# Optimization experiments

Measured on AMD Instinct MI355X. Metric: run time of the kernel, lower is better.

The kernel has to match this reference:

```python
import jax, jax.numpy as jnp
import numpy as np

B, LQ, LK, D = 16, 2048, 2048, 64
TEMPERATURE = 8.0


def setup_inputs() -> dict:
    key = jax.random.key(0)
    kq, kk, kv, kt, km = jax.random.split(key, 5)
    q = jax.random.normal(kq, (B, LQ, D), dtype=jnp.float32)
    k = jax.random.normal(kk, (B, LK, D), dtype=jnp.float32)
    v = jax.random.normal(kv, (B, LK, D), dtype=jnp.float32)
    # time differences are positive
    time_diff = jax.random.uniform(kt, (B, LQ, LK), dtype=jnp.float32)
    mask = jax.random.randint(km, (B, LQ, LK), 0, 2).astype(bool)
    time_plus_weight = jnp.zeros((1,), dtype=jnp.float32)
    time_mul_weight = jnp.ones((1,), dtype=jnp.float32)
    return {"q": q, "k": k, "v": v, "time_diff": time_diff, "mask": mask,
            "time_plus_weight": time_plus_weight, "time_mul_weight": time_mul_weight}


def reference(q, k, v, time_diff, mask, time_plus_weight, time_mul_weight):
    # attn = QK^T / temperature  -> [B, LQ, LK]
    attn = jnp.einsum("bqd,bkd->bqk", q, k) / TEMPERATURE
    # time-decay bias (global mean/max over the whole time_diff tensor)
    td = time_diff / jnp.mean(time_diff)
    td = td + jax.nn.softplus(time_plus_weight) * jnp.max(td)
    time_diff_weight = 1.0 / jnp.log(jnp.exp(jnp.float32(1.0)) + td)
    attn = attn + time_mul_weight * time_diff_weight
    attn = jnp.where(mask, jnp.float32(-1e10), attn)
    attn = jax.nn.softmax(attn, axis=2)
    # dropout is identity in eval / p-effective-0 reference
    output = jnp.einsum("bqk,bkd->bqd", attn, v)
    return (output, attn)
```

## Files before the change

kernel.cpp:

```cpp
#include <hip/hip_runtime.h>
#include <hip/hip_bf16.h>

#define B_N 16
#define LQ_N 2048
#define LK_N 2048
#define D_N 64

typedef __attribute__((ext_vector_type(8))) __bf16 bf16x8;
typedef __attribute__((ext_vector_type(4))) float f32x4;
typedef __attribute__((ext_vector_type(2))) unsigned u32x2;
typedef __attribute__((ext_vector_type(4))) unsigned u32x4;

__device__ __forceinline__ unsigned cvt_pk_bf16(float lo, float hi) {
  unsigned r;
  asm("v_cvt_pk_bf16_f32 %0, %1, %2" : "=v"(r) : "v"(lo), "v"(hi));
  return r;
}

__device__ __forceinline__ void gl_lds16(const float* g, float* l) {
  __builtin_amdgcn_global_load_lds(
      (const __attribute__((address_space(1))) void*)g,
      (__attribute__((address_space(3))) void*)l, 16, 0, 0);
}

#define WAIT_VMC(N)  do { asm volatile("s_waitcnt vmcnt(" #N ")" ::: "memory"); __builtin_amdgcn_sched_barrier(0); } while (0)
#define WAIT_LGKM0() do { asm volatile("s_waitcnt lgkmcnt(0)" ::: "memory");    __builtin_amdgcn_sched_barrier(0); } while (0)
#define SBAR()       __builtin_amdgcn_sched_barrier(0)

__global__ __launch_bounds__(256) void red1_kernel(const float* __restrict__ td,
                                                   float* __restrict__ ws) {
  const int tid = threadIdx.x;
  const int gid = blockIdx.x * 256 + tid;
  float s = 0.f, mx = -1e30f;
  const float4* p = reinterpret_cast<const float4*>(td);
  for (int i = gid; i < 16777216; i += 524288) {
    float4 x = p[i];
    s += (x.x + x.y) + (x.z + x.w);
    mx = fmaxf(mx, fmaxf(fmaxf(x.x, x.y), fmaxf(x.z, x.w)));
  }
#pragma unroll
  for (int m = 1; m < 64; m <<= 1) {
    s += __shfl_xor(s, m, 64);
    mx = fmaxf(mx, __shfl_xor(mx, m, 64));
  }
  __shared__ float ss[4], sm[4];
  if ((tid & 63) == 0) { ss[tid >> 6] = s; sm[tid >> 6] = mx; }
  __syncthreads();
  if (tid == 0) {
    ws[blockIdx.x]        = (ss[0] + ss[1]) + (ss[2] + ss[3]);
    ws[2048 + blockIdx.x] = fmaxf(fmaxf(sm[0], sm[1]), fmaxf(sm[2], sm[3]));
  }
}

__global__ __launch_bounds__(256) void red2_kernel(const float* __restrict__ tpw,
                                                   const unsigned* __restrict__ mku,
                                                   float* __restrict__ ws) {
  const int tid = threadIdx.x;
  double s = 0.0; float mx = -1e30f;
  for (int i = tid; i < 2048; i += 256) { s += (double)ws[i]; mx = fmaxf(mx, ws[2048 + i]); }
#pragma unroll
  for (int m = 1; m < 64; m <<= 1) {
    s += __shfl_xor(s, m, 64);
    mx = fmaxf(mx, __shfl_xor(mx, m, 64));
  }
  unsigned big = 0;
  for (int i = tid; i < 1024; i += 256) big |= (mku[i] > 1u) ? 1u : 0u;
  const int anyw = __any(big != 0);
  __shared__ double sd[4]; __shared__ float sm[4]; __shared__ int sa[4];
  if ((tid & 63) == 0) { sd[tid >> 6] = s; sm[tid >> 6] = mx; sa[tid >> 6] = anyw; }
  __syncthreads();
  if (tid == 0) {
    double tot = (sd[0] + sd[1]) + (sd[2] + sd[3]);
    float m4 = fmaxf(fmaxf(sm[0], sm[1]), fmaxf(sm[2], sm[3]));
    double mean = tot / 67108864.0;
    float inv_mean = (float)(1.0 / mean);
    float sp = log1pf(__expf(tpw[0]));
    ws[4096] = inv_mean;
    ws[4098] = (sa[0] | sa[1] | sa[2] | sa[3]) ? 1.f : 0.f;
    ws[4099] = 2.718281828459045f + sp * m4 * inv_mean;
  }
}

__global__ __launch_bounds__(512)
void attn_kernel(
    const float* __restrict__ q, const float* __restrict__ kp, const float* __restrict__ vp,
    const float* __restrict__ td, const unsigned char* __restrict__ maskb,
    const float* __restrict__ tmwp, const float* __restrict__ ws,
    float* __restrict__ out, float* __restrict__ attn) {

  __shared__ float regA[8][2][2048];
  __shared__ unsigned short Ps[8][16 * 40];
  __shared__ float rsum[8][16];

  const int tid  = threadIdx.x;
  const int w    = tid >> 6;
  const int lane = tid & 63;
  const int lrow = lane & 15;
  const int lgrp = lane >> 4;

  const int b     = blockIdx.x >> 7;
  const int qbase = (blockIdx.x & 127) << 4;

  const float inv_mean = ws[4096];
  const float ec       = ws[4099];
  const float tmw      = tmwp[0];
  const float sc       = tmw * 2.0813689810056077f;
  const int   msh      = (ws[4098] != 0.f) ? 0 : 2;

  const unsigned qrow = (unsigned)(b * LQ_N + qbase + lrow);
  const unsigned tdo0 = (qrow << 11) + (unsigned)(w * 32 + lgrp * 4);
  const unsigned kvo0 = ((unsigned)b << 17) + ((unsigned)w << 11);
  const unsigned pA = (lgrp << 6) + ((lrow ^ lgrp)       << 2);
  const unsigned pB = (lgrp << 6) + ((lrow ^ (lgrp + 4)) << 2);

  const float qscale = 0.18033688011112042f;
  bf16x8 qa[2];
  {
    const float* qb = q + ((size_t)qrow << 6) + lgrp * 8;
    f32x4 a0 = *reinterpret_cast<const f32x4*>(qb);
    f32x4 a1 = *reinterpret_cast<const f32x4*>(qb + 4);
    f32x4 a2 = *reinterpret_cast<const f32x4*>(qb + 32);
    f32x4 a3 = *reinterpret_cast<const f32x4*>(qb + 36);
    u32x4 k0 = { cvt_pk_bf16(a0[0]*qscale, a0[1]*qscale), cvt_pk_bf16(a0[2]*qscale, a0[3]*qscale),
                 cvt_pk_bf16(a1[0]*qscale, a1[1]*qscale), cvt_pk_bf16(a1[2]*qscale, a1[3]*qscale) };
    u32x4 k1 = { cvt_pk_bf16(a2[0]*qscale, a2[1]*qscale), cvt_pk_bf16(a2[2]*qscale, a2[3]*qscale),
                 cvt_pk_bf16(a3[0]*qscale, a3[1]*qscale), cvt_pk_bf16(a3[2]*qscale, a3[3]*qscale) };
    qa[0] = __builtin_bit_cast(bf16x8, k0);
    qa[1] = __builtin_bit_cast(bf16x8, k1);
  }

  auto dma = [&](const float* src_base, int c, int pb) {
    const unsigned base = kvo0 + (unsigned)c * 16384u;
#pragma unroll
    for (int t = 0; t < 8; ++t) {
      const unsigned perm = (t & 1) ? pB : pA;
      gl_lds16(src_base + (base + (unsigned)t * 256u + perm), &regA[w][pb][t * 256]);
    }
  };

  auto ldtd = [&](int c, f32x4* tdv, unsigned* mk4) {
    const unsigned to = tdo0 + (unsigned)c * 256u;
    tdv[0] = __builtin_nontemporal_load(reinterpret_cast<const f32x4*>(td + to));
    tdv[1] = __builtin_nontemporal_load(reinterpret_cast<const f32x4*>(td + to + 16));
    if (msh == 0) {
      mk4[0] = *reinterpret_cast<const unsigned*>(maskb + to);
      mk4[1] = *reinterpret_cast<const unsigned*>(maskb + to + 16);
    } else {
      u32x4 m0 = *reinterpret_cast<const u32x4*>(maskb + ((size_t)to << 2));
      u32x4 m1 = *reinterpret_cast<const u32x4*>(maskb + ((size_t)(to + 16u) << 2));
      mk4[0] = (m0[0] & 1u) | ((m0[1] & 1u) << 8) | ((m0[2] & 1u) << 16) | ((m0[3] & 1u) << 24);
      mk4[1] = (m1[0] & 1u) | ((m1[1] & 1u) << 8) | ((m1[2] & 1u) << 16) | ((m1[3] & 1u) << 24);
    }
  };

  dma(kp, 0, 0); SBAR();
  dma(kp, 1, 1); SBAR();
  f32x4    tdb[2][2];
  unsigned mkb[2][2];
  ldtd(0, tdb[0], mkb[0]); SBAR();

  float rs = 0.f;
  u32x2 E[8][2];

#pragma unroll
  for (int c = 0; c < 8; ++c) {
    if (c == 7) { WAIT_VMC(4); } else { WAIT_VMC(12); }

    const int x7 = lrow & 7;
    f32x4 acc0 = {0.f, 0.f, 0.f, 0.f};
    f32x4 acc1 = {0.f, 0.f, 0.f, 0.f};
#pragma unroll
    for (int T = 0; T < 2; ++T) {
      const int rr = T * 16 + lrow;
      f32x4 ka0 = *(const f32x4*)&regA[w][c & 1][rr * 64 + ((lgrp * 2    ) ^ x7) * 4];
      f32x4 ka1 = *(const f32x4*)&regA[w][c & 1][rr * 64 + ((lgrp * 2 + 1) ^ x7) * 4];
      f32x4 kb0 = *(const f32x4*)&regA[w][c & 1][rr * 64 + ((8 + lgrp * 2) ^ x7) * 4];
      f32x4 kb1 = *(const f32x4*)&regA[w][c & 1][rr * 64 + ((9 + lgrp * 2) ^ x7) * 4];
      u32x4 kd0 = { cvt_pk_bf16(ka0[0], ka0[1]), cvt_pk_bf16(ka0[2], ka0[3]),
                    cvt_pk_bf16(ka1[0], ka1[1]), cvt_pk_bf16(ka1[2], ka1[3]) };
      u32x4 kd1 = { cvt_pk_bf16(kb0[0], kb0[1]), cvt_pk_bf16(kb0[2], kb0[3]),
                    cvt_pk_bf16(kb1[0], kb1[1]), cvt_pk_bf16(kb1[2], kb1[3]) };
      f32x4& acc = (T == 0) ? acc0 : acc1;
      acc = __builtin_amdgcn_mfma_f32_16x16x32_bf16(__builtin_bit_cast(bf16x8, kd0), qa[0], acc, 0, 0, 0);
      acc = __builtin_amdgcn_mfma_f32_16x16x32_bf16(__builtin_bit_cast(bf16x8, kd1), qa[1], acc, 0, 0, 0);
    }
    WAIT_LGKM0();
    if (c < 6) { dma(kp, c + 2, c & 1); SBAR(); }
    if (c < 7) { ldtd(c + 1, tdb[(c + 1) & 1], mkb[(c + 1) & 1]); SBAR(); }

    if (c <= 5)      { WAIT_VMC(12); }
    else if (c == 6) { WAIT_VMC(4);  }
    else             { WAIT_VMC(0);  }

#pragma unroll
    for (int T = 0; T < 2; ++T) {
      const f32x4    tv  = tdb[c & 1][T];
      const unsigned mk4 = mkb[c & 1][T];
      float e4[4];
#pragma unroll
      for (int i = 0; i < 4; ++i) {
        const f32x4& acc = (T == 0) ? *(f32x4*)&((T==0)?acc0:acc1) : *(f32x4*)&acc1;
        (void)acc;
        const float av = (T == 0) ? ((i==0)?acc0[0]:(i==1)?acc0[1]:(i==2)?acc0[2]:acc0[3])
                                  : ((i==0)?acc1[0]:(i==1)?acc1[1]:(i==2)?acc1[2]:acc1[3]);
        const float z  = __builtin_fmaf(tv[i], inv_mean, ec);
        const float l2 = __builtin_amdgcn_logf(z);
        const float r  = __builtin_amdgcn_rcpf(l2);
        const float sv = __builtin_fmaf(sc, r, av);
        const float e  = ((mk4 >> (8 * i)) & 0xffu) ? 0.f : __builtin_amdgcn_exp2f(sv);
        e4[i] = e;
        rs += e;
      }
      E[c][T] = u32x2{ cvt_pk_bf16(e4[0], e4[1]), cvt_pk_bf16(e4[2], e4[3]) };
    }
  }

  dma(vp, 0, 0); SBAR();
  dma(vp, 1, 1); SBAR();

  rs += __shfl_xor(rs, 16, 64);
  rs += __shfl_xor(rs, 32, 64);
  if (lgrp == 0) rsum[w][lrow] = rs;
  __syncthreads();
  float invl;
  {
    float s = 0.f;
#pragma unroll
    for (int w2 = 0; w2 < 8; ++w2) s += rsum[w2][lrow];
    invl = __fdividef(1.f, s);
  }

  f32x4 oacc[4];
#pragma unroll
  for (int n = 0; n < 4; ++n) oacc[n] = {0.f, 0.f, 0.f, 0.f};

#pragma unroll
  for (int c = 0; c < 8; ++c) {
    if (c == 0)      { WAIT_VMC(8);  }
    else if (c == 1) { WAIT_VMC(10); }
    else if (c == 7) { WAIT_VMC(4);  }
    else             { WAIT_VMC(12); }

    f32x4 pv0, pv1;
    {
      const unsigned e0 = E[c][0][0], e1 = E[c][0][1];
      const unsigned f0 = E[c][1][0], f1 = E[c][1][1];
      pv0[0] = __uint_as_float(e0 << 16)         * invl;
      pv0[1] = __uint_as_float(e0 & 0xffff0000u) * invl;
      pv0[2] = __uint_as_float(e1 << 16)         * invl;
      pv0[3] = __uint_as_float(e1 & 0xffff0000u) * invl;
      pv1[0] = __uint_as_float(f0 << 16)         * invl;
      pv1[1] = __uint_as_float(f0 & 0xffff0000u) * invl;
      pv1[2] = __uint_as_float(f1 << 16)         * invl;
      pv1[3] = __uint_as_float(f1 & 0xffff0000u) * invl;
    }

    *reinterpret_cast<u32x2*>(&Ps[w][lrow * 40 + lgrp * 4]) =
        u32x2{ cvt_pk_bf16(pv0[0], pv0[1]), cvt_pk_bf16(pv0[2], pv0[3]) };
    *reinterpret_cast<u32x2*>(&Ps[w][lrow * 40 + 16 + lgrp * 4]) =
        u32x2{ cvt_pk_bf16(pv1[0], pv1[1]), cvt_pk_bf16(pv1[2], pv1[3]) };

    const bf16x8 pa = *(const bf16x8*)&Ps[w][lrow * 40 + lgrp * 8];

#pragma unroll
    for (int n = 0; n < 4; ++n) {
      float vv[8];
#pragma unroll
      for (int e = 0; e < 8; ++e) {
        const int r    = lgrp * 8 + e;
        const int dcol = n * 16 + lrow;
        const int slot = (dcol >> 2) ^ (r & 7);
        vv[e] = regA[w][c & 1][r * 64 + slot * 4 + (dcol & 3)];
      }
      u32x4 vd = { cvt_pk_bf16(vv[0], vv[1]), cvt_pk_bf16(vv[2], vv[3]),
                   cvt_pk_bf16(vv[4], vv[5]), cvt_pk_bf16(vv[6], vv[7]) };
      oacc[n] = __builtin_amdgcn_mfma_f32_16x16x32_bf16(pa, __builtin_bit_cast(bf16x8, vd),
                                                        oacc[n], 0, 0, 0);
    }

    WAIT_LGKM0();
    if (c < 6) { dma(vp, c + 2, c & 1); SBAR(); }

    const unsigned to = tdo0 + (unsigned)c * 256u;
    __builtin_nontemporal_store(pv0, reinterpret_cast<f32x4*>(attn + to));
    __builtin_nontemporal_store(pv1, reinterpret_cast<f32x4*>(attn + to + 16));
  }

  __syncthreads();
#pragma unroll
  for (int n = 0; n < 4; ++n)
#pragma unroll
    for (int i = 0; i < 4; ++i)
      regA[w][0][(lgrp * 4 + i) * 64 + n * 16 + lrow] = oacc[n][i];
  __syncthreads();
  for (int i2 = tid; i2 < 1024; i2 += 512) {
    float s = 0.f;
#pragma unroll
    for (int w2 = 0; w2 < 8; ++w2) s += regA[w2][0][i2];
    out[((size_t)(b * LQ_N + qbase) << 6) + i2] = s;
  }
}

extern "C" void kernel_launch(void* const* d_in, const int* in_sizes, int n_in,
                              void* d_out, int out_size, void* d_ws, size_t ws_size,
                              hipStream_t stream) {
  const float* q   = (const float*)d_in[0];
  const float* k   = (const float*)d_in[1];
  const float* v   = (const float*)d_in[2];
  const float* td  = (const float*)d_in[3];
  const unsigned char* mask = (const unsigned char*)d_in[4];
  const float* tpw = (const float*)d_in[5];
  const float* tmw = (const float*)d_in[6];
  float* out  = (float*)d_out;
  float* attn = out + (size_t)B_N * LQ_N * D_N;
  float* wsf  = (float*)d_ws;

  red1_kernel<<<2048, 256, 0, stream>>>(td, wsf);
  red2_kernel<<<1, 256, 0, stream>>>(tpw, (const unsigned*)mask, wsf);
  attn_kernel<<<2048, 512, 0, stream>>>(q, k, v, td, mask, tmw, wsf, out, attn);
}
```

Baseline: 328.6 us.

## Process two 16-row query tiles per block to reuse K/V tiles

Each block now handles 32 query rows instead of 16, so every K and V chunk staged in LDS feeds two sets of MFMAs, and the grid is halved to 1024 blocks. This halves K/V global traffic and the LDS conversion work per query row. In exchange it raises register use (more accumulators, E buffers, td/mask prefetch) and leaves fewer blocks for the 256 CUs, which may reduce occupancy and latency hiding. The vmcnt wait counts are retuned for the larger number of outstanding loads.

```diff
diff --git a/kernel.cpp b/kernel.cpp
--- a/kernel.cpp
+++ b/kernel.cpp
@@ -90,7 +90,7 @@
 
   __shared__ float regA[8][2][2048];
   __shared__ unsigned short Ps[8][16 * 40];
-  __shared__ float rsum[8][16];
+  __shared__ float rsum[2][8][16];
 
   const int tid  = threadIdx.x;
   const int w    = tid >> 6;
@@ -98,8 +98,8 @@
   const int lrow = lane & 15;
   const int lgrp = lane >> 4;
 
-  const int b     = blockIdx.x >> 7;
-  const int qbase = (blockIdx.x & 127) << 4;
+  const int b     = blockIdx.x >> 6;
+  const int qbase = (blockIdx.x & 63) << 5;
 
   const float inv_mean = ws[4096];
   const float ec       = ws[4099];
@@ -107,16 +107,18 @@
   const float sc       = tmw * 2.0813689810056077f;
   const int   msh      = (ws[4098] != 0.f) ? 0 : 2;
 
-  const unsigned qrow = (unsigned)(b * LQ_N + qbase + lrow);
-  const unsigned tdo0 = (qrow << 11) + (unsigned)(w * 32 + lgrp * 4);
-  const unsigned kvo0 = ((unsigned)b << 17) + ((unsigned)w << 11);
+  const unsigned qrow0 = (unsigned)(b * LQ_N + qbase + lrow);
+  const unsigned tdo0  = (qrow0 << 11) + (unsigned)(w * 32 + lgrp * 4);
+  const unsigned tdo1  = tdo0 + (16u << 11);
+  const unsigned kvo0  = ((unsigned)b << 17) + ((unsigned)w << 11);
   const unsigned pA = (lgrp << 6) + ((lrow ^ lgrp)       << 2);
   const unsigned pB = (lgrp << 6) + ((lrow ^ (lgrp + 4)) << 2);
 
   const float qscale = 0.18033688011112042f;
-  bf16x8 qa[2];
-  {
-    const float* qb = q + ((size_t)qrow << 6) + lgrp * 8;
+  bf16x8 qa[2][2];
+#pragma unroll
+  for (int qt = 0; qt < 2; ++qt) {
+    const float* qb = q + ((size_t)(qrow0 + qt * 16) << 6) + lgrp * 8;
     f32x4 a0 = *reinterpret_cast<const f32x4*>(qb);
     f32x4 a1 = *reinterpret_cast<const f32x4*>(qb + 4);
     f32x4 a2 = *reinterpret_cast<const f32x4*>(qb + 32);
@@ -125,8 +127,8 @@
                  cvt_pk_bf16(a1[0]*qscale, a1[1]*qscale), cvt_pk_bf16(a1[2]*qscale, a1[3]*qscale) };
     u32x4 k1 = { cvt_pk_bf16(a2[0]*qscale, a2[1]*qscale), cvt_pk_bf16(a2[2]*qscale, a2[3]*qscale),
                  cvt_pk_bf16(a3[0]*qscale, a3[1]*qscale), cvt_pk_bf16(a3[2]*qscale, a3[3]*qscale) };
-    qa[0] = __builtin_bit_cast(bf16x8, k0);
-    qa[1] = __builtin_bit_cast(bf16x8, k1);
+    qa[qt][0] = __builtin_bit_cast(bf16x8, k0);
+    qa[qt][1] = __builtin_bit_cast(bf16x8, k1);
   }
 
   auto dma = [&](const float* src_base, int c, int pb) {
@@ -138,37 +140,44 @@
     }
   };
 
-  auto ldtd = [&](int c, f32x4* tdv, unsigned* mk4) {
-    const unsigned to = tdo0 + (unsigned)c * 256u;
-    tdv[0] = __builtin_nontemporal_load(reinterpret_cast<const f32x4*>(td + to));
-    tdv[1] = __builtin_nontemporal_load(reinterpret_cast<const f32x4*>(td + to + 16));
-    if (msh == 0) {
-      mk4[0] = *reinterpret_cast<const unsigned*>(maskb + to);
-      mk4[1] = *reinterpret_cast<const unsigned*>(maskb + to + 16);
-    } else {
-      u32x4 m0 = *reinterpret_cast<const u32x4*>(maskb + ((size_t)to << 2));
-      u32x4 m1 = *reinterpret_cast<const u32x4*>(maskb + ((size_t)(to + 16u) << 2));
-      mk4[0] = (m0[0] & 1u) | ((m0[1] & 1u) << 8) | ((m0[2] & 1u) << 16) | ((m0[3] & 1u) << 24);
-      mk4[1] = (m1[0] & 1u) | ((m1[1] & 1u) << 8) | ((m1[2] & 1u) << 16) | ((m1[3] & 1u) << 24);
+  auto ldtd = [&](int c, f32x4 (*tdv)[2], unsigned (*mkv)[2]) {
+#pragma unroll
+    for (int qt = 0; qt < 2; ++qt) {
+      const unsigned to = ((qt == 0) ? tdo0 : tdo1) + (unsigned)c * 256u;
+      tdv[qt][0] = __builtin_nontemporal_load(reinterpret_cast<const f32x4*>(td + to));
+      tdv[qt][1] = __builtin_nontemporal_load(reinterpret_cast<const f32x4*>(td + to + 16));
+      if (msh == 0) {
+        mkv[qt][0] = *reinterpret_cast<const unsigned*>(maskb + to);
+        mkv[qt][1] = *reinterpret_cast<const unsigned*>(maskb + to + 16);
+      } else {
+        u32x4 m0 = *reinterpret_cast<const u32x4*>(maskb + ((size_t)to << 2));
+        u32x4 m1 = *reinterpret_cast<const u32x4*>(maskb + ((size_t)(to + 16u) << 2));
+        mkv[qt][0] = (m0[0] & 1u) | ((m0[1] & 1u) << 8) | ((m0[2] & 1u) << 16) | ((m0[3] & 1u) << 24);
+        mkv[qt][1] = (m1[0] & 1u) | ((m1[1] & 1u) << 8) | ((m1[2] & 1u) << 16) | ((m1[3] & 1u) << 24);
+      }
     }
   };
 
   dma(kp, 0, 0); SBAR();
   dma(kp, 1, 1); SBAR();
-  f32x4    tdb[2][2];
-  unsigned mkb[2][2];
+  f32x4    tdb[2][2][2];
+  unsigned mkb[2][2][2];
   ldtd(0, tdb[0], mkb[0]); SBAR();
 
-  float rs = 0.f;
-  u32x2 E[8][2];
+  float rs0 = 0.f, rs1 = 0.f;
+  u32x2 E[8][2][2];
 
 #pragma unroll
   for (int c = 0; c < 8; ++c) {
-    if (c == 7) { WAIT_VMC(4); } else { WAIT_VMC(12); }
+    if (c == 7) { WAIT_VMC(8); } else { WAIT_VMC(16); }
 
     const int x7 = lrow & 7;
-    f32x4 acc0 = {0.f, 0.f, 0.f, 0.f};
-    f32x4 acc1 = {0.f, 0.f, 0.f, 0.f};
+    f32x4 acc[2][2];
+#pragma unroll
+    for (int T = 0; T < 2; ++T)
+#pragma unroll
+      for (int qt = 0; qt < 2; ++qt) acc[T][qt] = f32x4{0.f, 0.f, 0.f, 0.f};
+
 #pragma unroll
     for (int T = 0; T < 2; ++T) {
       const int rr = T * 16 + lrow;
@@ -180,71 +189,97 @@
                     cvt_pk_bf16(ka1[0], ka1[1]), cvt_pk_bf16(ka1[2], ka1[3]) };
       u32x4 kd1 = { cvt_pk_bf16(kb0[0], kb0[1]), cvt_pk_bf16(kb0[2], kb0[3]),
                     cvt_pk_bf16(kb1[0], kb1[1]), cvt_pk_bf16(kb1[2], kb1[3]) };
-      f32x4& acc = (T == 0) ? acc0 : acc1;
-      acc = __builtin_amdgcn_mfma_f32_16x16x32_bf16(__builtin_bit_cast(bf16x8, kd0), qa[0], acc, 0, 0, 0);
-      acc = __builtin_amdgcn_mfma_f32_16x16x32_bf16(__builtin_bit_cast(bf16x8, kd1), qa[1], acc, 0, 0, 0);
+#pragma unroll
+      for (int qt = 0; qt < 2; ++qt) {
+        acc[T][qt] = __builtin_amdgcn_mfma_f32_16x16x32_bf16(
+            __builtin_bit_cast(bf16x8, kd0), qa[qt][0], acc[T][qt], 0, 0, 0);
+        acc[T][qt] = __builtin_amdgcn_mfma_f32_16x16x32_bf16(
+            __builtin_bit_cast(bf16x8, kd1), qa[qt][1], acc[T][qt], 0, 0, 0);
+      }
     }
     WAIT_LGKM0();
+    if (c < 7) { ldtd(c + 1, tdb[(c + 1) & 1], mkb[(c + 1) & 1]); SBAR(); }
     if (c < 6) { dma(kp, c + 2, c & 1); SBAR(); }
-    if (c < 7) { ldtd(c + 1, tdb[(c + 1) & 1], mkb[(c + 1) & 1]); SBAR(); }
-
-    if (c <= 5)      { WAIT_VMC(12); }
-    else if (c == 6) { WAIT_VMC(4);  }
+
+    if (c == 0)      { WAIT_VMC(16); }
+    else if (c <= 5) { WAIT_VMC(24); }
+    else if (c == 6) { WAIT_VMC(16); }
     else             { WAIT_VMC(0);  }
 
 #pragma unroll
-    for (int T = 0; T < 2; ++T) {
-      const f32x4    tv  = tdb[c & 1][T];
-      const unsigned mk4 = mkb[c & 1][T];
-      float e4[4];
-#pragma unroll
-      for (int i = 0; i < 4; ++i) {
-        const f32x4& acc = (T == 0) ? *(f32x4*)&((T==0)?acc0:acc1) : *(f32x4*)&acc1;
-        (void)acc;
-        const float av = (T == 0) ? ((i==0)?acc0[0]:(i==1)?acc0[1]:(i==2)?acc0[2]:acc0[3])
-                                  : ((i==0)?acc1[0]:(i==1)?acc1[1]:(i==2)?acc1[2]:acc1[3]);
-        const float z  = __builtin_fmaf(tv[i], inv_mean, ec);
-        const float l2 = __builtin_amdgcn_logf(z);
-        const float r  = __builtin_amdgcn_rcpf(l2);
-        const float sv = __builtin_fmaf(sc, r, av);
-        const float e  = ((mk4 >> (8 * i)) & 0xffu) ? 0.f : __builtin_amdgcn_exp2f(sv);
-        e4[i] = e;
-        rs += e;
-      }
-      E[c][T] = u32x2{ cvt_pk_bf16(e4[0], e4[1]), cvt_pk_bf16(e4[2], e4[3]) };
+    for (int qt = 0; qt < 2; ++qt) {
+#pragma unroll
+      for (int T = 0; T < 2; ++T) {
+        const f32x4    tv  = tdb[c & 1][qt][T];
+        const unsigned mk4 = mkb[c & 1][qt][T];
+        float e4[4];
+#pragma unroll
+        for (int i = 0; i < 4; ++i) {
+          const float av = acc[T][qt][i];
+          const float z  = __builtin_fmaf(tv[i], inv_mean, ec);
+          const float l2 = __builtin_amdgcn_logf(z);
+          const float r  = __builtin_amdgcn_rcpf(l2);
+          const float sv = __builtin_fmaf(sc, r, av);
+          const float e  = ((mk4 >> (8 * i)) & 0xffu) ? 0.f : __builtin_amdgcn_exp2f(sv);
+          e4[i] = e;
+          if (qt == 0) rs0 += e; else rs1 += e;
+        }
+        E[c][qt][T] = u32x2{ cvt_pk_bf16(e4[0], e4[1]), cvt_pk_bf16(e4[2], e4[3]) };
+      }
     }
   }
 
   dma(vp, 0, 0); SBAR();
   dma(vp, 1, 1); SBAR();
 
-  rs += __shfl_xor(rs, 16, 64);
-  rs += __shfl_xor(rs, 32, 64);
-  if (lgrp == 0) rsum[w][lrow] = rs;
-  __syncthreads();
-  float invl;
+  rs0 += __shfl_xor(rs0, 16, 64);
+  rs0 += __shfl_xor(rs0, 32, 64);
+  rs1 += __shfl_xor(rs1, 16, 64);
+  rs1 += __shfl_xor(rs1, 32, 64);
+  if (lgrp == 0) { rsum[0][w][lrow] = rs0; rsum[1][w][lrow] = rs1; }
+  __syncthreads();
+  float invl0, invl1;
   {
-    float s = 0.f;
-#pragma unroll
-    for (int w2 = 0; w2 < 8; ++w2) s += rsum[w2][lrow];
-    invl = __fdividef(1.f, s);
-  }
-
-  f32x4 oacc[4];
-#pragma unroll
-  for (int n = 0; n < 4; ++n) oacc[n] = {0.f, 0.f, 0.f, 0.f};
+    float s0 = 0.f, s1 = 0.f;
+#pragma unroll
+    for (int w2 = 0; w2 < 8; ++w2) { s0 += rsum[0][w2][lrow]; s1 += rsum[1][w2][lrow]; }
+    invl0 = __fdividef(1.f, s0);
+    invl1 = __fdividef(1.f, s1);
+  }
+
+  f32x4 oacc0[4], oacc1[4];
+#pragma unroll
+  for (int n = 0; n < 4; ++n) { oacc0[n] = f32x4{0.f,0.f,0.f,0.f}; oacc1[n] = f32x4{0.f,0.f,0.f,0.f}; }
 
 #pragma unroll
   for (int c = 0; c < 8; ++c) {
     if (c == 0)      { WAIT_VMC(8);  }
-    else if (c == 1) { WAIT_VMC(10); }
-    else if (c == 7) { WAIT_VMC(4);  }
-    else             { WAIT_VMC(12); }
-
-    f32x4 pv0, pv1;
-    {
-      const unsigned e0 = E[c][0][0], e1 = E[c][0][1];
-      const unsigned f0 = E[c][1][0], f1 = E[c][1][1];
+    else if (c == 1) { WAIT_VMC(12); }
+    else if (c == 7) { WAIT_VMC(8);  }
+    else             { WAIT_VMC(16); }
+
+    u32x4 vd[4];
+#pragma unroll
+    for (int n = 0; n < 4; ++n) {
+      float vv[8];
+#pragma unroll
+      for (int e = 0; e < 8; ++e) {
+        const int r    = lgrp * 8 + e;
+        const int dcol = n * 16 + lrow;
+        const int slot = (dcol >> 2) ^ (r & 7);
+        vv[e] = regA[w][c & 1][r * 64 + slot * 4 + (dcol & 3)];
+      }
+      vd[n] = u32x4{ cvt_pk_bf16(vv[0], vv[1]), cvt_pk_bf16(vv[2], vv[3]),
+                     cvt_pk_bf16(vv[4], vv[5]), cvt_pk_bf16(vv[6], vv[7]) };
+    }
+
+    f32x4 pvs[2][2];
+#pragma unroll
+    for (int qt = 0; qt < 2; ++qt) {
+      const float invl = (qt == 0) ? invl0 : invl1;
+      const unsigned e0 = E[c][qt][0][0], e1 = E[c][qt][0][1];
+      const unsigned f0 = E[c][qt][1][0], f1 = E[c][qt][1][1];
+      f32x4 pv0, pv1;
       pv0[0] = __uint_as_float(e0 << 16)         * invl;
       pv0[1] = __uint_as_float(e0 & 0xffff0000u) * invl;
       pv0[2] = __uint_as_float(e1 << 16)         * invl;
@@ -253,47 +288,43 @@
       pv1[1] = __uint_as_float(f0 & 0xffff0000u) * invl;
       pv1[2] = __uint_as_float(f1 << 16)         * invl;
       pv1[3] = __uint_as_float(f1 & 0xffff0000u) * invl;
-    }
-
-    *reinterpret_cast<u32x2*>(&Ps[w][lrow * 40 + lgrp * 4]) =
-        u32x2{ cvt_pk_bf16(pv0[0], pv0[1]), cvt_pk_bf16(pv0[2], pv0[3]) };
-    *reinterpret_cast<u32x2*>(&Ps[w][lrow * 40 + 16 + lgrp * 4]) =
-        u32x2{ cvt_pk_bf16(pv1[0], pv1[1]), cvt_pk_bf16(pv1[2], pv1[3]) };
-
-    const bf16x8 pa = *(const bf16x8*)&Ps[w][lrow * 40 + lgrp * 8];
-
-#pragma unroll
-    for (int n = 0; n < 4; ++n) {
-      float vv[8];
-#pragma unroll
-      for (int e = 0; e < 8; ++e) {
-        const int r    = lgrp * 8 + e;
-        const int dcol = n * 16 + lrow;
-        const int slot = (dcol >> 2) ^ (r & 7);
-        vv[e] = regA[w][c & 1][r * 64 + slot * 4 + (dcol & 3)];
-      }
-      u32x4 vd = { cvt_pk_bf16(vv[0], vv[1]), cvt_pk_bf16(vv[2], vv[3]),
-                   cvt_pk_bf16(vv[4], vv[5]), cvt_pk_bf16(vv[6], vv[7]) };
-      oacc[n] = __builtin_amdgcn_mfma_f32_16x16x32_bf16(pa, __builtin_bit_cast(bf16x8, vd),
-                                                        oacc[n], 0, 0, 0);
+      pvs[qt][0] = pv0; pvs[qt][1] = pv1;
+
+      *reinterpret_cast<u32x2*>(&Ps[w][lrow * 40 + lgrp * 4]) =
+          u32x2{ cvt_pk_bf16(pv0[0], pv0[1]), cvt_pk_bf16(pv0[2], pv0[3]) };
+      *reinterpret_cast<u32x2*>(&Ps[w][lrow * 40 + 16 + lgrp * 4]) =
+          u32x2{ cvt_pk_bf16(pv1[0], pv1[1]), cvt_pk_bf16(pv1[2], pv1[3]) };
+      const bf16x8 pa = *(const bf16x8*)&Ps[w][lrow * 40 + lgrp * 8];
+
+#pragma unroll
+      for (int n = 0; n < 4; ++n) {
+        f32x4& oc = (qt == 0) ? oacc0[n] : oacc1[n];
+        oc = __builtin_amdgcn_mfma_f32_16x16x32_bf16(pa, __builtin_bit_cast(bf16x8, vd[n]),
+                                                     oc, 0, 0, 0);
+      }
     }
 
     WAIT_LGKM0();
     if (c < 6) { dma(vp, c + 2, c & 1); SBAR(); }
 
-    const unsigned to = tdo0 + (unsigned)c * 256u;
-    __builtin_nontemporal_store(pv0, reinterpret_cast<f32x4*>(attn + to));
-    __builtin_nontemporal_store(pv1, reinterpret_cast<f32x4*>(attn + to + 16));
+#pragma unroll
+    for (int qt = 0; qt < 2; ++qt) {
+      const unsigned to = ((qt == 0) ? tdo0 : tdo1) + (unsigned)c * 256u;
+      __builtin_nontemporal_store(pvs[qt][0], reinterpret_cast<f32x4*>(attn + to));
+      __builtin_nontemporal_store(pvs[qt][1], reinterpret_cast<f32x4*>(attn + to + 16));
+    }
   }
 
   __syncthreads();
 #pragma unroll
   for (int n = 0; n < 4; ++n)
 #pragma unroll
-    for (int i = 0; i < 4; ++i)
-      regA[w][0][(lgrp * 4 + i) * 64 + n * 16 + lrow] = oacc[n][i];
-  __syncthreads();
-  for (int i2 = tid; i2 < 1024; i2 += 512) {
+    for (int i = 0; i < 4; ++i) {
+      regA[w][0][(lgrp * 4 + i) * 64 + n * 16 + lrow]        = oacc0[n][i];
+      regA[w][0][1024 + (lgrp * 4 + i) * 64 + n * 16 + lrow] = oacc1[n][i];
+    }
+  __syncthreads();
+  for (int i2 = tid; i2 < 2048; i2 += 512) {
     float s = 0.f;
 #pragma unroll
     for (int w2 = 0; w2 < 8; ++w2) s += regA[w2][0][i2];
@@ -317,5 +348,5 @@
 
   red1_kernel<<<2048, 256, 0, stream>>>(td, wsf);
   red2_kernel<<<1, 256, 0, stream>>>(tpw, (const unsigned*)mask, wsf);
-  attn_kernel<<<2048, 512, 0, stream>>>(q, k, v, td, mask, tmw, wsf, out, attn);
-}
+  attn_kernel<<<1024, 512, 0, stream>>>(q, k, v, td, mask, tmw, wsf, out, attn);
+}
```

Result: slower. 441.4 us (+34.3%).
